# Optimization experiments

Measured on AMD Instinct MI355X. Metric: run time of the kernel, lower is better.

## Reference

```python
import jax, jax.numpy as jnp
import numpy as np

B, S, D_MODEL, FILTER, K, MAX_FRAMES = 16, 512, 512, 512, 3, 2048


def _conv1d(x, w, b):
    # x: [B, C, L], w: [O, I, K], padding=1 -> same length
    y = jax.lax.conv_general_dilated(x, w, window_strides=(1,), padding=[(1, 1)],
                                     dimension_numbers=("NCH", "OIH", "NCH"))
    return y + b[None, :, None]


def _predictor(x, w1, b1, w2, b2, wl, bl):
    # x: [B, L, d] -> scalar track [B, L]
    h = x.transpose(0, 2, 1)                      # [B, d, L]
    h = jax.nn.relu(_conv1d(h, w1, b1))
    h = jax.nn.relu(_conv1d(h, w2, b2))
    h = h.transpose(0, 2, 1)                      # [B, L, filter]
    return (jnp.einsum("blf,f->bl", h, wl[:, 0]) + bl[0])


def _expand_hidden(H, D, max_T):
    # Length regulator: cumsum + searchsorted gather (vectorized repeat_interleave).
    D = jnp.maximum(D, 0).astype(jnp.int32)
    csum = jnp.cumsum(D, axis=1)                  # [B, S]
    t = jnp.arange(max_T, dtype=jnp.int32)        # [T]
    # idx[b, t] = # of cumsum entries <= t  == source token index for frame t
    idx = jax.vmap(lambda c: jnp.searchsorted(c, t, side="right"))(csum)  # [B, T]
    total = csum[:, -1]                           # [B]
    valid = t[None, :] < jnp.minimum(total, max_T)[:, None]               # [B, T]
    idx_safe = jnp.minimum(idx, S - 1)
    He = jnp.take_along_axis(H, idx_safe[:, :, None], axis=1)             # [B, T, d]
    return jnp.where(valid[:, :, None], He, jnp.zeros((), He.dtype))


def setup_inputs() -> dict:
    key = jax.random.key(0)
    ks = jax.random.split(key, 24)
    def w(k, shape, scale=0.05):
        return jax.random.normal(k, shape, dtype=jnp.float32) * scale
    inp = {
        "H": jax.random.normal(ks[0], (B, S, D_MODEL), dtype=jnp.float32),
        "D_gt": jax.random.randint(ks[1], (B, S), 0, 12, dtype=jnp.int32),
        "P_gt": jax.random.normal(ks[2], (B, MAX_FRAMES), dtype=jnp.float32),
        "E_gt": jax.random.normal(ks[3], (B, MAX_FRAMES), dtype=jnp.float32),
    }
    for i, p in enumerate(["dp", "pp", "ep"]):
        kk = jax.random.split(ks[4 + i], 3)
        inp[p + "_w1"] = w(kk[0], (FILTER, D_MODEL, K))
        inp[p + "_b1"] = jnp.zeros((FILTER,), jnp.float32)
        inp[p + "_w2"] = w(kk[1], (FILTER, FILTER, K))
        inp[p + "_b2"] = jnp.zeros((FILTER,), jnp.float32)
        inp[p + "_wl"] = w(kk[2], (FILTER, 1))
        inp[p + "_bl"] = jnp.zeros((1,), jnp.float32)
    inp["pitch_w"] = w(ks[8], (D_MODEL,))
    inp["pitch_b"] = jnp.zeros((D_MODEL,), jnp.float32)
    inp["energy_w"] = w(ks[9], (D_MODEL,))
    inp["energy_b"] = jnp.zeros((D_MODEL,), jnp.float32)
    return inp


def reference(H, D_gt, P_gt, E_gt,
              dp_w1, dp_b1, dp_w2, dp_b2, dp_wl, dp_bl,
              pp_w1, pp_b1, pp_w2, pp_b2, pp_wl, pp_bl,
              ep_w1, ep_b1, ep_w2, ep_b2, ep_wl, ep_bl,
              pitch_w, pitch_b, energy_w, energy_b):
    # Training path (is_inference=False): D = D_gt, P = P_gt, E = E_gt.
    D_pred = _predictor(H, dp_w1, dp_b1, dp_w2, dp_b2, dp_wl, dp_bl)     # [B, S]
    H_exp = _expand_hidden(H, D_gt, MAX_FRAMES)                           # [B, T, d]
    P_pred = _predictor(H_exp, pp_w1, pp_b1, pp_w2, pp_b2, pp_wl, pp_bl)  # [B, T]
    E_pred = _predictor(H_exp, ep_w1, ep_b1, ep_w2, ep_b2, ep_wl, ep_bl)  # [B, T]
    P_proj = P_gt[:, :, None] * pitch_w[None, None, :] + pitch_b          # Linear(1,d)
    E_proj = E_gt[:, :, None] * energy_w[None, None, :] + energy_b
    H_adapted = H_exp + P_proj + E_proj
    return (H_adapted, D_pred, P_pred, E_pred)
```

## Files before the change

### kernel.cpp

```cpp
#include <hip/hip_runtime.h>

#define B_ 16
#define S_ 512
#define C_ 512
#define T_ 2048

typedef __attribute__((ext_vector_type(8))) short short8;
typedef __attribute__((ext_vector_type(4))) float floatx4;

__device__ __forceinline__ unsigned short f2bf(float x) {
    union { float f; unsigned u; } c; c.f = x;
    unsigned r = (c.u + 0x7fffu + ((c.u >> 16) & 1u)) >> 16;
    return (unsigned short)r;
}

__device__ __forceinline__ void gld_lds16(void* l, const void* g) {
    __builtin_amdgcn_global_load_lds(
        (const __attribute__((address_space(1))) void*)g,
        (__attribute__((address_space(3))) void*)l, 16, 0, 0);
}

__global__ void prep_kernel(const float* __restrict__ w0, const float* __restrict__ w1,
                            const float* __restrict__ w2, const float* __restrict__ w3,
                            const float* __restrict__ w4, const float* __restrict__ w5,
                            unsigned short* __restrict__ wpack,
                            const float* __restrict__ H, unsigned short* __restrict__ Hbf,
                            unsigned short* __restrict__ zrow,
                            const int* __restrict__ Dgt, int* __restrict__ ridx,
                            float* __restrict__ Dp, float* __restrict__ Pp, float* __restrict__ Ep,
                            const float* __restrict__ dbl, const float* __restrict__ pbl,
                            const float* __restrict__ ebl) {
    __shared__ int cs[S_];
    __shared__ int ps[256];
    int blk = blockIdx.x;
    int tid = threadIdx.x;
    if (blk < 6144) {
        int which = blk >> 10;
        const float* w = which == 0 ? w0 : which == 1 ? w1 : which == 2 ? w2
                       : which == 3 ? w3 : which == 4 ? w4 : w5;
        unsigned short* wp = wpack + (long)which * 786432;
        int i = (blk & 1023) * 256 + tid;
        const float* s = w + (long)i * 3;
        wp[i]          = f2bf(s[0]);
        wp[i + 262144] = f2bf(s[1]);
        wp[i + 524288] = f2bf(s[2]);
    } else if (blk < 10240) {
        int i = (blk - 6144) * 256 + tid;
        float4 v = *(const float4*)(H + (long)i * 4);
        ushort4 o;
        o.x = f2bf(v.x); o.y = f2bf(v.y); o.z = f2bf(v.z); o.w = f2bf(v.w);
        *(ushort4*)(Hbf + (long)i * 4) = o;
    } else if (blk < 10242) {
        zrow[(blk - 10240) * 256 + tid] = 0;
    } else if (blk < 10258) {
        int b = blk - 10242;
        int t2 = tid * 2;
        int d0 = Dgt[b * S_ + t2], d1 = Dgt[b * S_ + t2 + 1];
        int a0 = d0 < 0 ? 0 : d0, a1 = d1 < 0 ? 0 : d1;
        ps[tid] = a0 + a1;
        __syncthreads();
        for (int off = 1; off < 256; off <<= 1) {
            int v = (tid >= off) ? ps[tid - off] : 0;
            __syncthreads();
            ps[tid] += v;
            __syncthreads();
        }
        int incl = ps[tid];
        cs[t2] = incl - a1;
        cs[t2 + 1] = incl;
        __syncthreads();
        int total = cs[S_ - 1];
        int limit = total < T_ ? total : T_;
        for (int t = tid; t < T_; t += 256) {
            int lo = 0, hi = S_;
            while (lo < hi) { int mid = (lo + hi) >> 1; if (cs[mid] <= t) lo = mid + 1; else hi = mid; }
            if (lo > S_ - 1) lo = S_ - 1;
            ridx[b * T_ + t] = (t < limit) ? lo : -1;
        }
    } else {
        int i = (blk - 10258) * 256 + tid;
        if (i < 8192) Dp[i] = dbl[0];
        else if (i < 40960) Pp[i - 8192] = pbl[0];
        else Ep[i - 40960] = ebl[0];
    }
}

struct ConvJob {
    const unsigned short* X;
    const int* ridx;
    int Lshift;
    int Bshift;
    const unsigned short* wp;
    const float* bias;
    const float* wl;
    void* dst;
    int nxshift;
};

template <int TAP>
__device__ __forceinline__ void compute_kt(
    floatx4 (&acc)[4][8],
    const unsigned short* Wb, const unsigned short* Xb,
    int wm, int wn, int q, int lr)
{
    short8 bfr[8];
    const int sX = ((lr + TAP) >> 1) & 3;
#pragma unroll
    for (int jj = 0; jj < 8; ++jj) {
        const int xr = wn * 128 + jj * 16 + lr + TAP;
        bfr[jj] = *(const short8*)(Xb + xr * 32 + ((q ^ sX) * 8));
    }
    const int sA = (lr >> 1) & 3;
#pragma unroll
    for (int i = 0; i < 4; ++i) {
        const int rA = wm * 64 + i * 16 + lr;
        short8 a = *(const short8*)(Wb + rA * 32 + ((q ^ sA) * 8));
#pragma unroll
        for (int jj = 0; jj < 8; ++jj)
            acc[i][jj] = __builtin_amdgcn_mfma_f32_16x16x32_bf16(a, bfr[jj], acc[i][jj], 0, 0, 0);
    }
}

#define VMWAIT(n) do { \
    asm volatile("s_waitcnt vmcnt(" #n ")" ::: "memory"); \
    __builtin_amdgcn_sched_barrier(0); \
    __builtin_amdgcn_s_barrier(); \
    __builtin_amdgcn_sched_barrier(0); \
} while (0)

__global__ __launch_bounds__(256, 2) void mega_kernel(
    ConvJob j0, ConvJob j1, ConvJob j2, int e0, int e1, int e2, int mode, int aoff,
    const unsigned short* __restrict__ zrow,
    const float* __restrict__ H, const int* __restrict__ aridx,
    const float* __restrict__ Pgt, const float* __restrict__ Egt,
    const float* __restrict__ pw, const float* __restrict__ pb,
    const float* __restrict__ ew, const float* __restrict__ eb,
    float* __restrict__ aout)
{
    extern __shared__ unsigned short lds[];
    const int bx = blockIdx.x;
    const int tid = threadIdx.x;

    if (bx >= e2) {
        int ab = bx - e2 + aoff;
#pragma unroll
        for (int it = 0; it < 8; ++it) {
            int i = ab * 256 + tid + it * 524288;
            int f4 = i & 127;
            int p  = i >> 7;
            int b  = p >> 11;
            int r  = aridx[p];
            float pg = Pgt[p], eg = Egt[p];
            int f = f4 << 2;
            float4 pwv = *(const float4*)(pw + f);
            float4 pbv = *(const float4*)(pb + f);
            float4 ewv = *(const float4*)(ew + f);
            float4 ebv = *(const float4*)(eb + f);
            float4 h = make_float4(0.f, 0.f, 0.f, 0.f);
            if (r >= 0) h = *(const float4*)(H + ((long)b * S_ + r) * C_ + f);
            float4 o;
            o.x = h.x + pg * pwv.x + pbv.x + eg * ewv.x + ebv.x;
            o.y = h.y + pg * pwv.y + pbv.y + eg * ewv.y + ebv.y;
            o.z = h.z + pg * pwv.z + pbv.z + eg * ewv.z + ebv.z;
            o.w = h.w + pg * pwv.w + pbv.w + eg * ewv.w + ebv.w;
            *(float4*)(aout + (long)p * C_ + f) = o;
        }
        return;
    }

    ConvJob j;
    int local;
    if (bx < e0)      { j = j0; local = bx; }
    else if (bx < e1) { j = j1; local = bx - e0; }
    else              { j = j2; local = bx - e1; }
    const int m0 = (local >> j.nxshift) * 128;
    const int n0 = (local & ((1 << j.nxshift) - 1)) * 256;
    const int L = 1 << j.Lshift;
    const int b = n0 >> j.Lshift;
    const int t0 = n0 & (L - 1);

    unsigned short* WtS = lds;
    unsigned short* XtS = lds + 8192;
    char* WtB = (char*)WtS;
    char* XtB = (char*)XtS;

    const int w = tid >> 6, l = tid & 63;
    const int q = l >> 4, lr = l & 15;
    const int wm = w & 1, wn = w >> 1;

    floatx4 acc[4][8];
#pragma unroll
    for (int i = 0; i < 4; ++i)
#pragma unroll
        for (int jj = 0; jj < 8; ++jj) acc[i][jj] = (floatx4){0.f, 0.f, 0.f, 0.f};

    const int sw = (((tid & 3) ^ ((tid >> 3) & 3))) * 8;
    auto xrowp = [&](int r) -> const unsigned short* {
        int t = t0 - 1 + r;
        if (t < 0 || t >= L) return zrow;
        int rr = j.ridx ? j.ridx[(b << j.Lshift) + t] : t;
        if (rr < 0) return zrow;
        return j.X + ((long)(b << j.Bshift) + rr) * C_;
    };
    const unsigned short* wsrc[2];
    const unsigned short* xsrc[4];
#pragma unroll
    for (int qq = 0; qq < 2; ++qq)
        wsrc[qq] = j.wp + (long)(m0 + qq * 64 + (tid >> 2)) * C_ + sw;
#pragma unroll
    for (int qq = 0; qq < 4; ++qq)
        xsrc[qq] = xrowp(qq * 64 + (tid >> 2)) + sw;
    const int ch_e = w * 2 + (l & 1);
    const unsigned short* xsrcE = xrowp(256 + (ch_e >> 2)) + (ch_e & 3) * 8;

    auto issueW = [&](int buf, int koff) {
        gld_lds16(WtB + buf * 8192 + 0 * 4096 + w * 1024, wsrc[0] + koff);
        gld_lds16(WtB + buf * 8192 + 1 * 4096 + w * 1024, wsrc[1] + koff);
    };
    auto issueX = [&](int buf, int xoff) {
        gld_lds16(XtB + buf * 16512 + 0 * 4096 + w * 1024, xsrc[0] + xoff);
        gld_lds16(XtB + buf * 16512 + 1 * 4096 + w * 1024, xsrc[1] + xoff);
        gld_lds16(XtB + buf * 16512 + 2 * 4096 + w * 1024, xsrc[2] + xoff);
        gld_lds16(XtB + buf * 16512 + 3 * 4096 + w * 1024, xsrc[3] + xoff);
        if (l < 2)
            gld_lds16(XtB + buf * 16512 + 16384 + w * 32, xsrcE + xoff);
    };

    issueX(0, 0);
    issueW(0, 0);

#pragma unroll 1
    for (int cc = 0; cc < 16; ++cc) {
        const int xb = cc & 1;
        const unsigned short* Xb = XtS + xb * 8256;
        const unsigned short* W0 = WtS + xb * 4096;
        const unsigned short* W1 = WtS + (xb ^ 1) * 4096;
        const int kW1 = 262144 + cc * 32;
        const int kW2 = 524288 + cc * 32;
        const int kW0n = cc * 32 + 32;
        const int xoffn = cc * 32 + 32;
        const bool more = (cc < 15);

        VMWAIT(0);
        issueW(xb ^ 1, kW1);
        compute_kt<0>(acc, W0, Xb, wm, wn, q, lr);

        VMWAIT(0);
        issueW(xb, kW2);
        if (more) issueX(xb ^ 1, xoffn);
        compute_kt<1>(acc, W1, Xb, wm, wn, q, lr);

        if (more) { VMWAIT(5); } else { VMWAIT(0); }
        if (more) issueW(xb ^ 1, kW0n);
        compute_kt<2>(acc, W0, Xb, wm, wn, q, lr);
    }

    const int fbase = m0 + wm * 64 + q * 4;
    const int pbase = n0 + wn * 128 + lr;
    if (mode == 0) {
        unsigned short* dst = (unsigned short*)j.dst;
#pragma unroll
        for (int i = 0; i < 4; ++i) {
            int f = fbase + i * 16;
            float4 bv = *(const float4*)(j.bias + f);
#pragma unroll
            for (int jj = 0; jj < 8; ++jj) {
                int p = pbase + jj * 16;
                ushort4 o;
                o.x = f2bf(fmaxf(acc[i][jj][0] + bv.x, 0.f));
                o.y = f2bf(fmaxf(acc[i][jj][1] + bv.y, 0.f));
                o.z = f2bf(fmaxf(acc[i][jj][2] + bv.z, 0.f));
                o.w = f2bf(fmaxf(acc[i][jj][3] + bv.w, 0.f));
                *(ushort4*)(dst + (long)p * C_ + f) = o;
            }
        }
    } else {
        float* dst = (float*)j.dst;
#pragma unroll
        for (int jj = 0; jj < 8; ++jj) {
            float s = 0.f;
#pragma unroll
            for (int i = 0; i < 4; ++i) {
                int f = fbase + i * 16;
                float4 bv = *(const float4*)(j.bias + f);
                float4 wv = *(const float4*)(j.wl + f);
                s += fmaxf(acc[i][jj][0] + bv.x, 0.f) * wv.x;
                s += fmaxf(acc[i][jj][1] + bv.y, 0.f) * wv.y;
                s += fmaxf(acc[i][jj][2] + bv.z, 0.f) * wv.z;
                s += fmaxf(acc[i][jj][3] + bv.w, 0.f) * wv.w;
            }
            s += __shfl_xor(s, 16, 64);
            s += __shfl_xor(s, 32, 64);
            if (l < 16) atomicAdd(dst + pbase + jj * 16, s);
        }
    }
}

extern "C" void kernel_launch(void* const* d_in, const int* in_sizes, int n_in,
                              void* d_out, int out_size, void* d_ws, size_t ws_size,
                              hipStream_t stream) {
    const float* H    = (const float*)d_in[0];
    const int*   Dgt  = (const int*)d_in[1];
    const float* Pgt  = (const float*)d_in[2];
    const float* Egt  = (const float*)d_in[3];
    const float* dp_w1 = (const float*)d_in[4];
    const float* dp_b1 = (const float*)d_in[5];
    const float* dp_w2 = (const float*)d_in[6];
    const float* dp_b2 = (const float*)d_in[7];
    const float* dp_wl = (const float*)d_in[8];
    const float* dp_bl = (const float*)d_in[9];
    const float* pp_w1 = (const float*)d_in[10];
    const float* pp_b1 = (const float*)d_in[11];
    const float* pp_w2 = (const float*)d_in[12];
    const float* pp_b2 = (const float*)d_in[13];
    const float* pp_wl = (const float*)d_in[14];
    const float* pp_bl = (const float*)d_in[15];
    const float* ep_w1 = (const float*)d_in[16];
    const float* ep_b1 = (const float*)d_in[17];
    const float* ep_w2 = (const float*)d_in[18];
    const float* ep_b2 = (const float*)d_in[19];
    const float* ep_wl = (const float*)d_in[20];
    const float* ep_bl = (const float*)d_in[21];
    const float* pitch_w  = (const float*)d_in[22];
    const float* pitch_b  = (const float*)d_in[23];
    const float* energy_w = (const float*)d_in[24];
    const float* energy_b = (const float*)d_in[25];

    float* out     = (float*)d_out;
    float* H_adapt = out;
    float* D_pred  = out + 16777216;
    float* P_pred  = out + 16785408;
    float* E_pred  = out + 16818176;

    const bool par = ws_size >= 94000000ull;

    char* ws = (char*)d_ws;
    size_t off = 0;
    unsigned short* wpack = (unsigned short*)(ws + off); off += 6UL * 786432UL * 2UL;
    unsigned short* Hbf   = (unsigned short*)(ws + off); off += 4194304UL * 2UL;
    unsigned short* h1a   = (unsigned short*)(ws + off); off += 16777216UL * 2UL;
    unsigned short* h1b   = par ? (unsigned short*)(ws + off) : h1a;
    if (par) off += 16777216UL * 2UL;
    unsigned short* h1dp  = (unsigned short*)(ws + off); off += 4194304UL * 2UL;
    unsigned short* zrow  = (unsigned short*)(ws + off); off += 512UL * 2UL;
    off = (off + 255) & ~(size_t)255;
    int* ridx_exp = (int*)(ws + off); off += (size_t)B_ * T_ * 4;

    hipLaunchKernelGGL(prep_kernel, dim3(10546), dim3(256), 0, stream,
                       dp_w1, dp_w2, pp_w1, pp_w2, ep_w1, ep_w2, wpack, H, Hbf, zrow,
                       Dgt, ridx_exp, D_pred, P_pred, E_pred, dp_bl, pp_bl, ep_bl);

    ConvJob j_pp1 = { Hbf,  ridx_exp, 11,  9, wpack + 2UL * 786432, pp_b1, nullptr, h1a,    7 };
    ConvJob j_ep1 = { Hbf,  ridx_exp, 11,  9, wpack + 4UL * 786432, ep_b1, nullptr, h1b,    7 };
    ConvJob j_dp1 = { Hbf,  nullptr,   9,  9, wpack + 0UL * 786432, dp_b1, nullptr, h1dp,   5 };
    ConvJob j_pp2 = { h1a,  nullptr,  11, 11, wpack + 3UL * 786432, pp_b2, pp_wl,  P_pred, 7 };
    ConvJob j_ep2 = { h1b,  nullptr,  11, 11, wpack + 5UL * 786432, ep_b2, ep_wl,  E_pred, 7 };
    ConvJob j_dp2 = { h1dp, nullptr,   9,  9, wpack + 1UL * 786432, dp_b2, dp_wl,  D_pred, 5 };

    const unsigned lds_bytes = 49408;

    if (par) {
        hipLaunchKernelGGL(mega_kernel, dim3(1152 + 1024), dim3(256), lds_bytes, stream,
                           j_pp1, j_ep1, j_dp1, 512, 1024, 1152, 0, 0, zrow,
                           H, ridx_exp, Pgt, Egt, pitch_w, pitch_b, energy_w, energy_b, H_adapt);
        hipLaunchKernelGGL(mega_kernel, dim3(1152 + 1024), dim3(256), lds_bytes, stream,
                           j_pp2, j_ep2, j_dp2, 512, 1024, 1152, 1, 1024, zrow,
                           H, ridx_exp, Pgt, Egt, pitch_w, pitch_b, energy_w, energy_b, H_adapt);
    } else {
        hipLaunchKernelGGL(mega_kernel, dim3(640 + 2048), dim3(256), lds_bytes, stream,
                           j_pp1, j_dp1, j_dp1, 512, 640, 640, 0, 0, zrow,
                           H, ridx_exp, Pgt, Egt, pitch_w, pitch_b, energy_w, energy_b, H_adapt);
        hipLaunchKernelGGL(mega_kernel, dim3(640), dim3(256), lds_bytes, stream,
                           j_pp2, j_dp2, j_dp2, 512, 640, 640, 1, 0, zrow,
                           H, ridx_exp, Pgt, Egt, pitch_w, pitch_b, energy_w, energy_b, H_adapt);
        hipLaunchKernelGGL(mega_kernel, dim3(512), dim3(256), lds_bytes, stream,
                           j_ep1, j_ep1, j_ep1, 512, 512, 512, 0, 0, zrow,
                           H, ridx_exp, Pgt, Egt, pitch_w, pitch_b, energy_w, energy_b, H_adapt);
        hipLaunchKernelGGL(mega_kernel, dim3(512), dim3(256), lds_bytes, stream,
                           j_ep2, j_ep2, j_ep2, 512, 512, 512, 1, 0, zrow,
                           H, ridx_exp, Pgt, Egt, pitch_w, pitch_b, energy_w, energy_b, H_adapt);
    }
}
```

Measured before the change: 344.6 us.

## Double conv tile width to 512 positions with 512-thread blocks and all-tap prefetch

Widens the conv GEMM block tile from 128x256 to 128x512 output positions and launches 512 threads per block. All three weight taps plus the next X slab are now prefetched into a double-buffered LDS layout, so each k-step needs one barrier instead of three. The goal is more reuse of each loaded weight tile and fewer synchronisations. The cost is roughly 115 KB of LDS per block, which means one block per CU and about half as many blocks, so occupancy and load balance may drop.

```diff
diff --git a/kernel.cpp b/kernel.cpp
--- a/kernel.cpp
+++ b/kernel.cpp
@@ -128,7 +128,7 @@
     __builtin_amdgcn_sched_barrier(0); \
 } while (0)
 
-__global__ __launch_bounds__(256, 2) void mega_kernel(
+__global__ __launch_bounds__(512, 2) void mega_kernel(
     ConvJob j0, ConvJob j1, ConvJob j2, int e0, int e1, int e2, int mode, int aoff,
     const unsigned short* __restrict__ zrow,
     const float* __restrict__ H, const int* __restrict__ aridx,
@@ -145,7 +145,7 @@
         int ab = bx - e2 + aoff;
 #pragma unroll
         for (int it = 0; it < 8; ++it) {
-            int i = ab * 256 + tid + it * 524288;
+            int i = ab * 512 + tid + it * 524288;
             int f4 = i & 127;
             int p  = i >> 7;
             int b  = p >> 11;
@@ -174,13 +174,13 @@
     else if (bx < e1) { j = j1; local = bx - e0; }
     else              { j = j2; local = bx - e1; }
     const int m0 = (local >> j.nxshift) * 128;
-    const int n0 = (local & ((1 << j.nxshift) - 1)) * 256;
+    const int n0 = (local & ((1 << j.nxshift) - 1)) * 512;
     const int L = 1 << j.Lshift;
     const int b = n0 >> j.Lshift;
     const int t0 = n0 & (L - 1);
 
     unsigned short* WtS = lds;
-    unsigned short* XtS = lds + 8192;
+    unsigned short* XtS = lds + 24576;
     char* WtB = (char*)WtS;
     char* XtB = (char*)XtS;
 
@@ -202,57 +202,46 @@
         if (rr < 0) return zrow;
         return j.X + ((long)(b << j.Bshift) + rr) * C_;
     };
-    const unsigned short* wsrc[2];
+    const unsigned short* wsrcT[3];
+#pragma unroll
+    for (int tap = 0; tap < 3; ++tap)
+        wsrcT[tap] = j.wp + (long)tap * 262144 + (long)(m0 + (tid >> 2)) * C_ + sw;
     const unsigned short* xsrc[4];
 #pragma unroll
-    for (int qq = 0; qq < 2; ++qq)
-        wsrc[qq] = j.wp + (long)(m0 + qq * 64 + (tid >> 2)) * C_ + sw;
-#pragma unroll
     for (int qq = 0; qq < 4; ++qq)
-        xsrc[qq] = xrowp(qq * 64 + (tid >> 2)) + sw;
-    const int ch_e = w * 2 + (l & 1);
-    const unsigned short* xsrcE = xrowp(256 + (ch_e >> 2)) + (ch_e & 3) * 8;
-
-    auto issueW = [&](int buf, int koff) {
-        gld_lds16(WtB + buf * 8192 + 0 * 4096 + w * 1024, wsrc[0] + koff);
-        gld_lds16(WtB + buf * 8192 + 1 * 4096 + w * 1024, wsrc[1] + koff);
+        xsrc[qq] = xrowp(qq * 128 + (tid >> 2)) + sw;
+    const unsigned short* xsrcE = xrowp(512 + (tid >> 2)) + (tid & 3) * 8;
+
+    auto issueW = [&](int par, int tap, int koff) {
+        gld_lds16(WtB + (par * 3 + tap) * 8192 + w * 1024, wsrcT[tap] + koff);
     };
-    auto issueX = [&](int buf, int xoff) {
-        gld_lds16(XtB + buf * 16512 + 0 * 4096 + w * 1024, xsrc[0] + xoff);
-        gld_lds16(XtB + buf * 16512 + 1 * 4096 + w * 1024, xsrc[1] + xoff);
-        gld_lds16(XtB + buf * 16512 + 2 * 4096 + w * 1024, xsrc[2] + xoff);
-        gld_lds16(XtB + buf * 16512 + 3 * 4096 + w * 1024, xsrc[3] + xoff);
-        if (l < 2)
-            gld_lds16(XtB + buf * 16512 + 16384 + w * 32, xsrcE + xoff);
+    auto issueX = [&](int par, int xoff) {
+        gld_lds16(XtB + par * 32896 + 0 * 8192 + w * 1024, xsrc[0] + xoff);
+        gld_lds16(XtB + par * 32896 + 1 * 8192 + w * 1024, xsrc[1] + xoff);
+        gld_lds16(XtB + par * 32896 + 2 * 8192 + w * 1024, xsrc[2] + xoff);
+        gld_lds16(XtB + par * 32896 + 3 * 8192 + w * 1024, xsrc[3] + xoff);
+        if (tid < 8)
+            gld_lds16(XtB + par * 32896 + 32768, xsrcE + xoff);
     };
 
     issueX(0, 0);
-    issueW(0, 0);
+    issueW(0, 0, 0); issueW(0, 1, 0); issueW(0, 2, 0);
 
 #pragma unroll 1
     for (int cc = 0; cc < 16; ++cc) {
-        const int xb = cc & 1;
-        const unsigned short* Xb = XtS + xb * 8256;
-        const unsigned short* W0 = WtS + xb * 4096;
-        const unsigned short* W1 = WtS + (xb ^ 1) * 4096;
-        const int kW1 = 262144 + cc * 32;
-        const int kW2 = 524288 + cc * 32;
-        const int kW0n = cc * 32 + 32;
-        const int xoffn = cc * 32 + 32;
-        const bool more = (cc < 15);
-
+        const int par = cc & 1;
         VMWAIT(0);
-        issueW(xb ^ 1, kW1);
-        compute_kt<0>(acc, W0, Xb, wm, wn, q, lr);
-
-        VMWAIT(0);
-        issueW(xb, kW2);
-        if (more) issueX(xb ^ 1, xoffn);
-        compute_kt<1>(acc, W1, Xb, wm, wn, q, lr);
-
-        if (more) { VMWAIT(5); } else { VMWAIT(0); }
-        if (more) issueW(xb ^ 1, kW0n);
-        compute_kt<2>(acc, W0, Xb, wm, wn, q, lr);
+        if (cc < 15) {
+            const int np = par ^ 1;
+            const int ko = (cc + 1) * 32;
+            issueW(np, 0, ko); issueW(np, 1, ko); issueW(np, 2, ko);
+            issueX(np, ko);
+        }
+        const unsigned short* Wp = WtS + par * 12288;
+        const unsigned short* Xb = XtS + par * 16448;
+        compute_kt<0>(acc, Wp,        Xb, wm, wn, q, lr);
+        compute_kt<1>(acc, Wp + 4096, Xb, wm, wn, q, lr);
+        compute_kt<2>(acc, Wp + 8192, Xb, wm, wn, q, lr);
     }
 
     const int fbase = m0 + wm * 64 + q * 4;
@@ -350,34 +339,34 @@
                        dp_w1, dp_w2, pp_w1, pp_w2, ep_w1, ep_w2, wpack, H, Hbf, zrow,
                        Dgt, ridx_exp, D_pred, P_pred, E_pred, dp_bl, pp_bl, ep_bl);
 
-    ConvJob j_pp1 = { Hbf,  ridx_exp, 11,  9, wpack + 2UL * 786432, pp_b1, nullptr, h1a,    7 };
-    ConvJob j_ep1 = { Hbf,  ridx_exp, 11,  9, wpack + 4UL * 786432, ep_b1, nullptr, h1b,    7 };
-    ConvJob j_dp1 = { Hbf,  nullptr,   9,  9, wpack + 0UL * 786432, dp_b1, nullptr, h1dp,   5 };
-    ConvJob j_pp2 = { h1a,  nullptr,  11, 11, wpack + 3UL * 786432, pp_b2, pp_wl,  P_pred, 7 };
-    ConvJob j_ep2 = { h1b,  nullptr,  11, 11, wpack + 5UL * 786432, ep_b2, ep_wl,  E_pred, 7 };
-    ConvJob j_dp2 = { h1dp, nullptr,   9,  9, wpack + 1UL * 786432, dp_b2, dp_wl,  D_pred, 5 };
-
-    const unsigned lds_bytes = 49408;
+    ConvJob j_pp1 = { Hbf,  ridx_exp, 11,  9, wpack + 2UL * 786432, pp_b1, nullptr, h1a,    6 };
+    ConvJob j_ep1 = { Hbf,  ridx_exp, 11,  9, wpack + 4UL * 786432, ep_b1, nullptr, h1b,    6 };
+    ConvJob j_dp1 = { Hbf,  nullptr,   9,  9, wpack + 0UL * 786432, dp_b1, nullptr, h1dp,   4 };
+    ConvJob j_pp2 = { h1a,  nullptr,  11, 11, wpack + 3UL * 786432, pp_b2, pp_wl,  P_pred, 6 };
+    ConvJob j_ep2 = { h1b,  nullptr,  11, 11, wpack + 5UL * 786432, ep_b2, ep_wl,  E_pred, 6 };
+    ConvJob j_dp2 = { h1dp, nullptr,   9,  9, wpack + 1UL * 786432, dp_b2, dp_wl,  D_pred, 4 };
+
+    const unsigned lds_bytes = 114944;
 
     if (par) {
-        hipLaunchKernelGGL(mega_kernel, dim3(1152 + 1024), dim3(256), lds_bytes, stream,
-                           j_pp1, j_ep1, j_dp1, 512, 1024, 1152, 0, 0, zrow,
-                           H, ridx_exp, Pgt, Egt, pitch_w, pitch_b, energy_w, energy_b, H_adapt);
-        hipLaunchKernelGGL(mega_kernel, dim3(1152 + 1024), dim3(256), lds_bytes, stream,
-                           j_pp2, j_ep2, j_dp2, 512, 1024, 1152, 1, 1024, zrow,
+        hipLaunchKernelGGL(mega_kernel, dim3(576 + 512), dim3(512), lds_bytes, stream,
+                           j_pp1, j_ep1, j_dp1, 256, 512, 576, 0, 0, zrow,
+                           H, ridx_exp, Pgt, Egt, pitch_w, pitch_b, energy_w, energy_b, H_adapt);
+        hipLaunchKernelGGL(mega_kernel, dim3(576 + 512), dim3(512), lds_bytes, stream,
+                           j_pp2, j_ep2, j_dp2, 256, 512, 576, 1, 512, zrow,
                            H, ridx_exp, Pgt, Egt, pitch_w, pitch_b, energy_w, energy_b, H_adapt);
     } else {
-        hipLaunchKernelGGL(mega_kernel, dim3(640 + 2048), dim3(256), lds_bytes, stream,
-                           j_pp1, j_dp1, j_dp1, 512, 640, 640, 0, 0, zrow,
-                           H, ridx_exp, Pgt, Egt, pitch_w, pitch_b, energy_w, energy_b, H_adapt);
-        hipLaunchKernelGGL(mega_kernel, dim3(640), dim3(256), lds_bytes, stream,
-                           j_pp2, j_dp2, j_dp2, 512, 640, 640, 1, 0, zrow,
-                           H, ridx_exp, Pgt, Egt, pitch_w, pitch_b, energy_w, energy_b, H_adapt);
-        hipLaunchKernelGGL(mega_kernel, dim3(512), dim3(256), lds_bytes, stream,
-                           j_ep1, j_ep1, j_ep1, 512, 512, 512, 0, 0, zrow,
-                           H, ridx_exp, Pgt, Egt, pitch_w, pitch_b, energy_w, energy_b, H_adapt);
-        hipLaunchKernelGGL(mega_kernel, dim3(512), dim3(256), lds_bytes, stream,
-                           j_ep2, j_ep2, j_ep2, 512, 512, 512, 1, 0, zrow,
-                           H, ridx_exp, Pgt, Egt, pitch_w, pitch_b, energy_w, energy_b, H_adapt);
-    }
-}
+        hipLaunchKernelGGL(mega_kernel, dim3(320 + 1024), dim3(512), lds_bytes, stream,
+                           j_pp1, j_dp1, j_dp1, 256, 320, 320, 0, 0, zrow,
+                           H, ridx_exp, Pgt, Egt, pitch_w, pitch_b, energy_w, energy_b, H_adapt);
+        hipLaunchKernelGGL(mega_kernel, dim3(320), dim3(512), lds_bytes, stream,
+                           j_pp2, j_dp2, j_dp2, 256, 320, 320, 1, 0, zrow,
+                           H, ridx_exp, Pgt, Egt, pitch_w, pitch_b, energy_w, energy_b, H_adapt);
+        hipLaunchKernelGGL(mega_kernel, dim3(256), dim3(512), lds_bytes, stream,
+                           j_ep1, j_ep1, j_ep1, 256, 256, 256, 0, 0, zrow,
+                           H, ridx_exp, Pgt, Egt, pitch_w, pitch_b, energy_w, energy_b, H_adapt);
+        hipLaunchKernelGGL(mega_kernel, dim3(256), dim3(512), lds_bytes, stream,
+                           j_ep2, j_ep2, j_ep2, 256, 256, 256, 1, 0, zrow,
+                           H, ridx_exp, Pgt, Egt, pitch_w, pitch_b, energy_w, energy_b, H_adapt);
+    }
+}
```

After: 396.1 us. +14.9%, slower.
